# Kernel optimization log

Hardware: AMD Instinct MI355X
Metric: run time of the kernel (lower is better)

The kernel has to match this reference:

```python
import jax, jax.numpy as jnp
import numpy as np

N = 50000
E = 800000
NUM_GRAPHS = 128
X_IN, HID, EDGE_DIM = 64, 64, 16


def setup_inputs() -> dict:
    key = jax.random.key(0)
    ks = jax.random.split(key, 9)
    s = 0.05
    inp = {
        'x': jax.random.normal(ks[0], (N, X_IN), jnp.float32),
        'edge_index': jax.random.randint(ks[1], (2, E), 0, N, dtype=jnp.int32),
        'edge_attr': jax.random.normal(ks[2], (E, EDGE_DIM), jnp.float32),
        'batch': jnp.sort(jax.random.randint(ks[3], (N,), 0, NUM_GRAPHS, dtype=jnp.int32)),
        'w_fc1': jax.random.normal(ks[4], (EDGE_DIM, 1), jnp.float32) * s,
        'b_fc1': jnp.zeros((1,), jnp.float32),
    }
    dims = [(X_IN, HID), (HID, HID * 2), (HID * 2, HID)]
    for i, (din, dout) in enumerate(dims):
        k1, k2, k3 = jax.random.split(ks[5 + i], 3)
        inp[f'w1_{i}'] = jax.random.normal(k1, (din, dout), jnp.float32) * s
        inp[f'b1_{i}'] = jnp.zeros((dout,), jnp.float32)
        inp[f'w2_{i}'] = jax.random.normal(k2, (din, dout), jnp.float32) * s
        inp[f'w3_{i}'] = jax.random.normal(k3, (din, dout), jnp.float32) * s
        inp[f'b3_{i}'] = jnp.zeros((dout,), jnp.float32)
    return inp


def leconv(x, src, dst, ew, w1, b1, w2, w3, b3):
    # PyG LEConv: out_i = lin3(x_i) + sum_{j->i} e_ji * (lin1(x_j) - lin2(x_i))
    a = x @ w1 + b1          # lin1 (bias=True)   [N, out]
    b = x @ w2               # lin2 (bias=False)  [N, out]
    msg = ew[:, None] * (a[src] - b[dst])          # [E, out]
    agg = jax.ops.segment_sum(msg, dst, num_segments=N)
    return agg + x @ w3 + b3  # lin3 (bias=True)


def reference(x, edge_index, edge_attr, batch,
              w_fc1, b_fc1,
              w1_0, b1_0, w2_0, w3_0, b3_0,
              w1_1, b1_1, w2_1, w3_1, b3_1,
              w1_2, b1_2, w2_2, w3_2, b3_2):
    src, dst = edge_index[0], edge_index[1]
    ew = (edge_attr @ w_fc1 + b_fc1)[:, 0]         # fc1(edge_attr).squeeze(-1) -> [E]
    h = jax.nn.elu(leconv(x, src, dst, ew, w1_0, b1_0, w2_0, w3_0, b3_0))
    h = jax.nn.elu(leconv(h, src, dst, ew, w1_1, b1_1, w2_1, w3_1, b3_1))
    h = jax.nn.elu(leconv(h, src, dst, ew, w1_2, b1_2, w2_2, w3_2, b3_2))
    # global max pool over nodes of each graph -> [NUM_GRAPHS, HID]
    return jax.ops.segment_max(h, batch, num_segments=NUM_GRAPHS)
```

## Files before the change

### kernel.cpp

```cpp
#include <hip/hip_runtime.h>
#include <math.h>

#define N_NODES 50000
#define N_EDGES 800000
#define NUM_GRAPHS_ 128
#define SCAN_NB 98
#define NPASS 8
#define NODES_PER_PASS 6250
#define HCHUNKS 128
#define EDGES_PER_CHUNK 6250
#define HWORDS 12500
#define TS_BPH 196

typedef unsigned short u16;
typedef unsigned int u32;
typedef __attribute__((ext_vector_type(8))) short bf16x8;
typedef __attribute__((ext_vector_type(4))) float f32x4;

__device__ __forceinline__ float elu_f(float v) {
    return v > 0.f ? v : (__expf(v) - 1.f);
}
__device__ __forceinline__ u16 f2bf(float f) {
    u32 u = __float_as_uint(f);
    u += 0x7FFFu + ((u >> 16) & 1u);
    return (u16)(u >> 16);
}
__device__ __forceinline__ float bf2f(u16 h) {
    return __uint_as_float(((u32)h) << 16);
}
__device__ __forceinline__ void bfpair(u32 v, float& lo, float& hi) {
    lo = __uint_as_float(v << 16);
    hi = __uint_as_float(v & 0xFFFF0000u);
}
__device__ __forceinline__ u32 packbf(float lo, float hi) {
    return (u32)f2bf(lo) | ((u32)f2bf(hi) << 16);
}

__global__ void prep_kernel(const float* __restrict__ edge_attr,
                            const float* __restrict__ w_fc1,
                            const float* __restrict__ b_fc1,
                            const int* __restrict__ edge_index,
                            float* __restrict__ ew,
                            u16* __restrict__ dst16,
                            const float* __restrict__ x, u16* __restrict__ xb,
                            const float* __restrict__ w3_0, const float* __restrict__ w1_0, const float* __restrict__ w2_0,
                            const float* __restrict__ w3_1, const float* __restrict__ w1_1, const float* __restrict__ w2_1,
                            const float* __restrict__ w3_2, const float* __restrict__ w1_2, const float* __restrict__ w2_2,
                            u16* __restrict__ bp0, u16* __restrict__ bp1, u16* __restrict__ bp2) {
    const int b = blockIdx.x;
    if (b < 3125) {
        const int e = b * 256 + threadIdx.x;
        const float4* ea = (const float4*)(edge_attr + (size_t)e * 16);
        const float4* wf = (const float4*)w_fc1;
        float acc = b_fc1[0];
#pragma unroll
        for (int i = 0; i < 4; i++) {
            float4 a = ea[i], w = wf[i];
            acc += a.x * w.x + a.y * w.y + a.z * w.z + a.w * w.w;
        }
        ew[e] = acc;
        dst16[e] = (u16)edge_index[N_EDGES + e];
    } else if (b < 6250) {
        const int g = (b - 3125) * 256 + threadIdx.x;
        float4 v = ((const float4*)x)[g];
        uint2 o;
        o.x = packbf(v.x, v.y);
        o.y = packbf(v.z, v.w);
        ((uint2*)xb)[g] = o;
    } else {
        const int t = (b - 6250) * 256 + threadIdx.x;
        u16 buf[8];
        if (t < 4608) {
            int DOUT, lid;
            const float *w3, *w1, *w2;
            u16* bp;
            if (t < 1536) { DOUT = 64;  lid = t;        w3 = w3_0; w1 = w1_0; w2 = w2_0; bp = bp0; }
            else          { DOUT = 128; lid = t - 1536; w3 = w3_1; w1 = w1_1; w2 = w2_1; bp = bp1; }
            const int NT = DOUT / 16;
            const int lane = lid & 63;
            const int fragid = lid >> 6;
            const int chunk = fragid / NT;
            const int ntile = fragid % NT;
            const int n = ntile * 16 + (lane & 15);
            const int kbase = chunk * 32 + (lane >> 4) * 8;
#pragma unroll
            for (int j = 0; j < 8; j++) {
                int k = kbase + j;
                int region = k / 64;
                int kk = k - region * 64;
                float v = (region == 0) ? w3[kk * DOUT + n]
                        : (region == 1) ? w1[kk * DOUT + n]
                                        : -w2[kk * DOUT + n];
                buf[j] = f2bf(v);
            }
            *(bf16x8*)(bp + ((size_t)lid << 3)) = *(bf16x8*)buf;
        } else if (t < 7680) {
            const int lid = t - 4608;
            const int NT = 12;
            const int lane = lid & 63;
            const int fragid = lid >> 6;
            const int chunk = fragid / NT;
            const int ntile = fragid % NT;
            const int n = ntile * 16 + (lane & 15);
            const int kbase = chunk * 32 + (lane >> 4) * 8;
#pragma unroll
            for (int j = 0; j < 8; j++) {
                int k = kbase + j;
                float v = (n < 64)  ? w3_2[k * 64 + n]
                        : (n < 128) ? -w2_2[k * 64 + (n - 64)]
                                    : w1_2[k * 64 + (n - 128)];
                buf[j] = f2bf(v);
            }
            *(bf16x8*)(bp2 + ((size_t)lid << 3)) = *(bf16x8*)buf;
        }
    }
}

__global__ __launch_bounds__(256) void deg_hist_kernel(const u16* __restrict__ dst16,
                                                       u32* __restrict__ partial) {
    __shared__ u32 bins[HWORDS];
    const int c = blockIdx.x >> 1;
    const int p = blockIdx.x & 1;
    const int t = threadIdx.x;
    for (int i = t; i < HWORDS; i += 256) bins[i] = 0;
    __syncthreads();
    const int base = c * EDGES_PER_CHUNK;
    const int nlo = p * 25000;
    for (int i = t; i < EDGES_PER_CHUNK; i += 256) {
        const int b = (int)dst16[base + i] - nlo;
        if ((unsigned)b < 25000u)
            atomicAdd(&bins[b >> 1], 1u << ((b & 1) * 16));
    }
    __syncthreads();
    u32* outp = partial + (size_t)blockIdx.x * HWORDS;
    for (int i = t; i < HWORDS; i += 256) outp[i] = bins[i];
}

__global__ __launch_bounds__(256) void scan_chunks_kernel(const u32* __restrict__ partial,
                                                          u32* __restrict__ prefpack,
                                                          u32* __restrict__ degpack) {
    __shared__ u32 qsums[4][64];
    const int t = threadIdx.x;
    const int p = (blockIdx.x >= TS_BPH) ? 1 : 0;
    const int wh0 = (blockIdx.x - p * TS_BPH) << 6;
    const int wl = t & 63;
    const int cq = t >> 6;
    const int wh = wh0 + wl;
    const bool ok = wh < HWORDS;

    u32 vals[32];
#pragma unroll
    for (int i = 0; i < 32; i++) {
        const int c = cq * 32 + i;
        vals[i] = ok ? partial[(size_t)((c << 1) + p) * HWORDS + wh] : 0u;
    }
    u32 s = 0;
#pragma unroll
    for (int i = 0; i < 32; i++) s += vals[i];
    qsums[cq][wl] = s;
    __syncthreads();
    u32 run = 0;
#pragma unroll
    for (int j = 0; j < 4; j++)
        if (j < cq) run += qsums[j][wl];

    if (ok) {
        const int g = p * HWORDS + wh;
#pragma unroll
        for (int i = 0; i < 32; i++) {
            const int c = cq * 32 + i;
            prefpack[(size_t)c * 25000 + g] = run;
            run += vals[i];
        }
        if (cq == 3) degpack[g] = run;
    }
}

__global__ __launch_bounds__(256) void scan1_kernel(const u32* __restrict__ degpack,
                                                    int* __restrict__ rowptr,
                                                    int* __restrict__ blk_sums) {
    __shared__ int sh[256];
    const int t = threadIdx.x;
    const int base = blockIdx.x * 512;
    const int i0 = base + 2 * t, i1 = i0 + 1;
    int d0 = 0, d1 = 0;
    if (i0 < N_NODES) {
        u32 v = degpack[i0 >> 1];
        d0 = (int)(v & 0xFFFFu);
        d1 = (int)(v >> 16);
    }
    const int pair = d0 + d1;
    int v = pair;
    sh[t] = v;
    __syncthreads();
#pragma unroll
    for (int off = 1; off < 256; off <<= 1) {
        int add = (t >= off) ? sh[t - off] : 0;
        __syncthreads();
        v += add;
        sh[t] = v;
        __syncthreads();
    }
    const int excl = v - pair;
    if (i0 < N_NODES) rowptr[i0] = excl;
    if (i1 < N_NODES) rowptr[i1] = excl + d0;
    if (t == 255) blk_sums[blockIdx.x] = v;
}

__global__ __launch_bounds__(128) void scan2_kernel(const int* __restrict__ blk_sums,
                                                    int* __restrict__ blk_offs,
                                                    int* __restrict__ rowptr) {
    __shared__ int sh[128];
    const int t = threadIdx.x;
    const int orig = (t < SCAN_NB) ? blk_sums[t] : 0;
    int v = orig;
    sh[t] = v;
    __syncthreads();
#pragma unroll
    for (int off = 1; off < 128; off <<= 1) {
        int add = (t >= off) ? sh[t - off] : 0;
        __syncthreads();
        v += add;
        sh[t] = v;
        __syncthreads();
    }
    if (t < SCAN_NB) blk_offs[t] = v - orig;
    if (t == 127) rowptr[N_NODES] = v;
}

__global__ void scan3_kernel(int* __restrict__ rowptr,
                             const int* __restrict__ blk_offs) {
    int i = blockIdx.x * blockDim.x + threadIdx.x;
    if (i >= N_NODES) return;
    rowptr[i] += blk_offs[i >> 9];
}

__global__ __launch_bounds__(256) void place_kernel(const int* __restrict__ edge_index,
                                                    const float* __restrict__ ew,
                                                    const u16* __restrict__ dst16,
                                                    const int* __restrict__ rowptr,
                                                    const u32* __restrict__ prefpack,
                                                    int2* __restrict__ csr) {
    __shared__ int lcur[NODES_PER_PASS];
    const int pass = blockIdx.x & (NPASS - 1);
    const int c = blockIdx.x >> 3;
    const int lo = pass * NODES_PER_PASS;
    const int t = threadIdx.x;
    for (int i = t; i < NODES_PER_PASS; i += 256) lcur[i] = 0;
    __syncthreads();
    const int base = c * EDGES_PER_CHUNK;
    for (int i = t; i < EDGES_PER_CHUNK; i += 256) {
        const int e = base + i;
        const int d = (int)dst16[e];
        const int dl = d - lo;
        if ((unsigned)dl < (unsigned)NODES_PER_PASS) {
            u32 pw = prefpack[(size_t)c * 25000 + (d >> 1)];
            int pref = (int)((pw >> ((d & 1) * 16)) & 0xFFFFu);
            int lpos = atomicAdd(&lcur[dl], 1);
            int2 ent;
            ent.x = edge_index[e];
            ent.y = __float_as_int(ew[e]);
            csr[rowptr[d] + pref + lpos] = ent;
        }
    }
}

template <int DIN, bool WRITE_C>
__global__ __launch_bounds__(256) void gather_kernel(
    const u16* __restrict__ xb, const int* __restrict__ rowptr,
    const int2* __restrict__ csr, u16* __restrict__ sb,
    u16* __restrict__ chb, float* __restrict__ c) {
    constexpr int CG = DIN / 4;
    constexpr int EG = 64 / CG;
    const int gid = blockIdx.x * 256 + threadIdx.x;
    const int node = gid >> 6;
    if (node >= N_NODES) return;
    const int lane = threadIdx.x & 63;
    const int cg = lane & (CG - 1);
    const int eg = lane / CG;
    const int beg = rowptr[node];
    const int end = rowptr[node + 1];
    const uint2* x2 = (const uint2*)xb;

    float a0 = 0.f, a1 = 0.f, a2 = 0.f, a3 = 0.f;
    float b0 = 0.f, b1 = 0.f, b2 = 0.f, b3 = 0.f;
    float wsum = 0.f;

    int p = beg + eg;
    for (; p + EG < end; p += 2 * EG) {
        int2 e0 = csr[p];
        int2 e1 = csr[p + EG];
        float w0 = __int_as_float(e0.y);
        float w1 = __int_as_float(e1.y);
        uint2 v0 = x2[(size_t)e0.x * CG + cg];
        uint2 v1 = x2[(size_t)e1.x * CG + cg];
        float f0, f1, f2, f3, g0, g1, g2, g3;
        bfpair(v0.x, f0, f1); bfpair(v0.y, f2, f3);
        bfpair(v1.x, g0, g1); bfpair(v1.y, g2, g3);
        a0 += w0 * f0; a1 += w0 * f1; a2 += w0 * f2; a3 += w0 * f3;
        b0 += w1 * g0; b1 += w1 * g1; b2 += w1 * g2; b3 += w1 * g3;
        wsum += w0 + w1;
    }
    if (p < end) {
        int2 e0 = csr[p];
        float w0 = __int_as_float(e0.y);
        uint2 v0 = x2[(size_t)e0.x * CG + cg];
        float f0, f1, f2, f3;
        bfpair(v0.x, f0, f1); bfpair(v0.y, f2, f3);
        a0 += w0 * f0; a1 += w0 * f1; a2 += w0 * f2; a3 += w0 * f3;
        wsum += w0;
    }
    a0 += b0; a1 += b1; a2 += b2; a3 += b3;

#pragma unroll
    for (int off = 32; off >= CG; off >>= 1) {
        a0 += __shfl_xor(a0, off);
        a1 += __shfl_xor(a1, off);
        a2 += __shfl_xor(a2, off);
        a3 += __shfl_xor(a3, off);
        wsum += __shfl_xor(wsum, off);
    }

    if (lane < CG) {
        uint2 so;
        so.x = packbf(a0, a1);
        so.y = packbf(a2, a3);
        ((uint2*)sb)[(size_t)node * CG + cg] = so;
        const float cn = WRITE_C ? wsum : c[node];
        uint2 hv = x2[(size_t)node * CG + cg];
        float h0, h1, h2, h3;
        bfpair(hv.x, h0, h1); bfpair(hv.y, h2, h3);
        uint2 co;
        co.x = packbf(cn * h0, cn * h1);
        co.y = packbf(cn * h2, cn * h3);
        ((uint2*)chb)[(size_t)node * CG + cg] = co;
    }
    if (WRITE_C && lane == 0) c[node] = wsum;
}

template <int DIN, int DOUT>
__global__ __launch_bounds__(256) void gemm_mfma(
    const u16* __restrict__ hb, const u16* __restrict__ sb,
    const u16* __restrict__ chb, const u16* __restrict__ Bp,
    const float* __restrict__ cvec, const float* __restrict__ bias1,
    const float* __restrict__ bias3, u16* __restrict__ outp) {
    constexpr int CH = DIN / 32;
    constexpr int CHUNKS = 3 * CH;
    constexpr int NT = DOUT / 16;
    const int tid = threadIdx.x;
    const int wv = tid >> 6;
    const int lane = tid & 63;
    const int l15 = lane & 15;
    const int q = lane >> 4;
    const int mhalf = wv & 1;
    const int nhalf = wv >> 1;
    const int row_base = blockIdx.x * 64 + mhalf * 32;
    const int nt0 = blockIdx.y * 4 + nhalf * 2;

    const int r0 = min(row_base + l15, N_NODES - 1);
    const int r1 = min(row_base + 16 + l15, N_NODES - 1);
    const int qo = q * 8;

    f32x4 acc00 = {0.f, 0.f, 0.f, 0.f};
    f32x4 acc01 = {0.f, 0.f, 0.f, 0.f};
    f32x4 acc10 = {0.f, 0.f, 0.f, 0.f};
    f32x4 acc11 = {0.f, 0.f, 0.f, 0.f};

#pragma unroll
    for (int chunk = 0; chunk < CHUNKS; chunk++) {
        const int region = chunk / CH;
        const int koff = (chunk - region * CH) * 32 + qo;
        const u16* A = (region == 0) ? hb : (region == 1) ? sb : chb;
        bf16x8 a0 = *(const bf16x8*)(A + (size_t)r0 * DIN + koff);
        bf16x8 a1 = *(const bf16x8*)(A + (size_t)r1 * DIN + koff);
        const u16* bp = Bp + (((size_t)(chunk * NT + nt0) * 64 + lane) << 3);
        bf16x8 bf0 = *(const bf16x8*)bp;
        bf16x8 bf1 = *(const bf16x8*)(bp + 64 * 8);
        acc00 = __builtin_amdgcn_mfma_f32_16x16x32_bf16(a0, bf0, acc00, 0, 0, 0);
        acc01 = __builtin_amdgcn_mfma_f32_16x16x32_bf16(a0, bf1, acc01, 0, 0, 0);
        acc10 = __builtin_amdgcn_mfma_f32_16x16x32_bf16(a1, bf0, acc10, 0, 0, 0);
        acc11 = __builtin_amdgcn_mfma_f32_16x16x32_bf16(a1, bf1, acc11, 0, 0, 0);
    }

#pragma unroll
    for (int ni = 0; ni < 2; ni++) {
        const int col = (nt0 + ni) * 16 + l15;
        const float B3 = bias3[col];
        const float B1 = bias1[col];
        const f32x4 am0 = ni ? acc01 : acc00;
        const f32x4 am1 = ni ? acc11 : acc10;
#pragma unroll
        for (int mi = 0; mi < 2; mi++) {
            const f32x4 av = mi ? am1 : am0;
#pragma unroll
            for (int reg = 0; reg < 4; reg++) {
                const int row = row_base + mi * 16 + q * 4 + reg;
                if (row < N_NODES) {
                    const float cv = cvec[row];
                    const float val = av[reg] + B3 + cv * B1;
                    outp[(size_t)row * DOUT + col] = f2bf(elu_f(val));
                }
            }
        }
    }
}

__global__ __launch_bounds__(256) void gemm_l1_fused(
    const u16* __restrict__ hb, const u16* __restrict__ sb,
    const u16* __restrict__ chb, const u16* __restrict__ Bp1,
    const u16* __restrict__ Bp2, const float* __restrict__ cvec,
    const float* __restrict__ bias1, const float* __restrict__ bias3,
    u16* __restrict__ zuy) {
    __shared__ u16 ht[64][136];
    const int tid = threadIdx.x;
    const int wv = tid >> 6;
    const int lane = tid & 63;
    const int l15 = lane & 15;
    const int q = lane >> 4;
    const int mhalf = wv & 1;
    const int nhalf = wv >> 1;
    const int row_base = blockIdx.x * 64 + mhalf * 32;
    const int r0 = min(row_base + l15, N_NODES - 1);
    const int r1 = min(row_base + 16 + l15, N_NODES - 1);
    const int qo = q * 8;

    {
        const int nt0 = nhalf * 4;
        f32x4 acc[2][4] = {};
#pragma unroll
        for (int chunk = 0; chunk < 6; chunk++) {
            const int region = chunk / 2;
            const int koff = (chunk - region * 2) * 32 + qo;
            const u16* A = (region == 0) ? hb : (region == 1) ? sb : chb;
            bf16x8 a0 = *(const bf16x8*)(A + (size_t)r0 * 64 + koff);
            bf16x8 a1 = *(const bf16x8*)(A + (size_t)r1 * 64 + koff);
#pragma unroll
            for (int ni = 0; ni < 4; ni++) {
                bf16x8 bf = *(const bf16x8*)(Bp1 + (((size_t)(chunk * 8 + nt0 + ni) * 64 + lane) << 3));
                acc[0][ni] = __builtin_amdgcn_mfma_f32_16x16x32_bf16(a0, bf, acc[0][ni], 0, 0, 0);
                acc[1][ni] = __builtin_amdgcn_mfma_f32_16x16x32_bf16(a1, bf, acc[1][ni], 0, 0, 0);
            }
        }
#pragma unroll
        for (int ni = 0; ni < 4; ni++) {
            const int col = (nt0 + ni) * 16 + l15;
            const float B3 = bias3[col];
            const float B1 = bias1[col];
#pragma unroll
            for (int mi = 0; mi < 2; mi++) {
#pragma unroll
                for (int reg = 0; reg < 4; reg++) {
                    const int lrow = mhalf * 32 + mi * 16 + q * 4 + reg;
                    const int grow = blockIdx.x * 64 + lrow;
                    const float cv = cvec[min(grow, N_NODES - 1)];
                    ht[lrow][col] = f2bf(elu_f(acc[mi][ni][reg] + B3 + cv * B1));
                }
            }
        }
    }
    __syncthreads();

    {
        const int nt2 = nhalf * 6;
        f32x4 acc[2][6] = {};
#pragma unroll
        for (int chunk = 0; chunk < 4; chunk++) {
            const int koff = chunk * 32 + qo;
            bf16x8 a0 = *(const bf16x8*)(&ht[mhalf * 32 + l15][koff]);
            bf16x8 a1 = *(const bf16x8*)(&ht[mhalf * 32 + 16 + l15][koff]);
#pragma unroll
            for (int ni = 0; ni < 6; ni++) {
                bf16x8 bf = *(const bf16x8*)(Bp2 + (((size_t)(chunk * 12 + nt2 + ni) * 64 + lane) << 3));
                acc[0][ni] = __builtin_amdgcn_mfma_f32_16x16x32_bf16(a0, bf, acc[0][ni], 0, 0, 0);
                acc[1][ni] = __builtin_amdgcn_mfma_f32_16x16x32_bf16(a1, bf, acc[1][ni], 0, 0, 0);
            }
        }
#pragma unroll
        for (int ni = 0; ni < 6; ni++) {
            const int col = (nt2 + ni) * 16 + l15;
#pragma unroll
            for (int mi = 0; mi < 2; mi++) {
#pragma unroll
                for (int reg = 0; reg < 4; reg++) {
                    const int row = row_base + mi * 16 + q * 4 + reg;
                    if (row < N_NODES)
                        zuy[(size_t)row * 192 + col] = f2bf(acc[mi][ni][reg]);
                }
            }
        }
    }
}

__global__ __launch_bounds__(256) void gather2_kernel(
    const u16* __restrict__ zuy, const int* __restrict__ rowptr,
    const int2* __restrict__ csr, const float* __restrict__ c,
    const float* __restrict__ bias1, const float* __restrict__ bias3,
    u16* __restrict__ h3) {
    constexpr int CG = 16, EG = 4;
    const int gid = blockIdx.x * 256 + threadIdx.x;
    const int node = gid >> 6;
    if (node >= N_NODES) return;
    const int lane = threadIdx.x & 63;
    const int cg = lane & (CG - 1);
    const int eg = lane >> 4;
    const int beg = rowptr[node];
    const int end = rowptr[node + 1];

    float a0 = 0.f, a1 = 0.f, a2 = 0.f, a3 = 0.f;
    float b0 = 0.f, b1 = 0.f, b2 = 0.f, b3 = 0.f;

    int p = beg + eg;
    for (; p + EG < end; p += 2 * EG) {
        int2 e0 = csr[p];
        int2 e1 = csr[p + EG];
        float w0 = __int_as_float(e0.y);
        float w1 = __int_as_float(e1.y);
        uint2 v0 = ((const uint2*)(zuy + (size_t)e0.x * 192 + 128))[cg];
        uint2 v1 = ((const uint2*)(zuy + (size_t)e1.x * 192 + 128))[cg];
        float f0, f1, f2, f3, g0, g1, g2, g3;
        bfpair(v0.x, f0, f1); bfpair(v0.y, f2, f3);
        bfpair(v1.x, g0, g1); bfpair(v1.y, g2, g3);
        a0 += w0 * f0; a1 += w0 * f1; a2 += w0 * f2; a3 += w0 * f3;
        b0 += w1 * g0; b1 += w1 * g1; b2 += w1 * g2; b3 += w1 * g3;
    }
    if (p < end) {
        int2 e0 = csr[p];
        float w0 = __int_as_float(e0.y);
        uint2 v0 = ((const uint2*)(zuy + (size_t)e0.x * 192 + 128))[cg];
        float f0, f1, f2, f3;
        bfpair(v0.x, f0, f1); bfpair(v0.y, f2, f3);
        a0 += w0 * f0; a1 += w0 * f1; a2 += w0 * f2; a3 += w0 * f3;
    }
    a0 += b0; a1 += b1; a2 += b2; a3 += b3;

#pragma unroll
    for (int off = 32; off >= CG; off >>= 1) {
        a0 += __shfl_xor(a0, off);
        a1 += __shfl_xor(a1, off);
        a2 += __shfl_xor(a2, off);
        a3 += __shfl_xor(a3, off);
    }

    if (lane < CG) {
        const float cn = c[node];
        const u16* zr = zuy + (size_t)node * 192;
        uint2 zv = ((const uint2*)zr)[cg];
        uint2 uv = ((const uint2*)(zr + 64))[cg];
        float z0, z1, z2, z3, u0, u1, u2, u3;
        bfpair(zv.x, z0, z1); bfpair(zv.y, z2, z3);
        bfpair(uv.x, u0, u1); bfpair(uv.y, u2, u3);
        const float4 b3v = *(const float4*)(bias3 + cg * 4);
        const float4 b1v = *(const float4*)(bias1 + cg * 4);
        float o0 = elu_f(z0 + cn * u0 + a0 + b3v.x + cn * b1v.x);
        float o1 = elu_f(z1 + cn * u1 + a1 + b3v.y + cn * b1v.y);
        float o2 = elu_f(z2 + cn * u2 + a2 + b3v.z + cn * b1v.z);
        float o3 = elu_f(z3 + cn * u3 + a3 + b3v.w + cn * b1v.w);
        uint2 o;
        o.x = packbf(o0, o1);
        o.y = packbf(o2, o3);
        ((uint2*)h3)[(size_t)node * CG + cg] = o;
    }
}

__global__ void pool_kernel(const u16* __restrict__ h,
                            const int* __restrict__ batch,
                            float* __restrict__ out) {
    const int g = blockIdx.x;
    const int tid = threadIdx.x;
    int lo = 0, hi = N_NODES;
    while (lo < hi) { int mid = (lo + hi) >> 1; if (batch[mid] < g) lo = mid + 1; else hi = mid; }
    const int beg = lo;
    lo = beg; hi = N_NODES;
    while (lo < hi) { int mid = (lo + hi) >> 1; if (batch[mid] < g + 1) lo = mid + 1; else hi = mid; }
    const int end = lo;

    __shared__ float red[256];
    const int col = tid & 63;
    const int rg = tid >> 6;
    float m = -3.0e38f;
    for (int r = beg + rg; r < end; r += 4) m = fmaxf(m, bf2f(h[(size_t)r * 64 + col]));
    red[tid] = m;
    __syncthreads();
    if (tid < 64) {
        m = fmaxf(fmaxf(red[tid], red[tid + 64]), fmaxf(red[tid + 128], red[tid + 192]));
        out[g * 64 + tid] = m;
    }
}

extern "C" void kernel_launch(void* const* d_in, const int* in_sizes, int n_in,
                              void* d_out, int out_size, void* d_ws, size_t ws_size,
                              hipStream_t stream) {
    const float* x = (const float*)d_in[0];
    const int* ei = (const int*)d_in[1];
    const float* ea = (const float*)d_in[2];
    const int* batch = (const int*)d_in[3];
    const float* wfc = (const float*)d_in[4];
    const float* bfc = (const float*)d_in[5];
    const float* w1_0 = (const float*)d_in[6];
    const float* b1_0 = (const float*)d_in[7];
    const float* w2_0 = (const float*)d_in[8];
    const float* w3_0 = (const float*)d_in[9];
    const float* b3_0 = (const float*)d_in[10];
    const float* w1_1 = (const float*)d_in[11];
    const float* b1_1 = (const float*)d_in[12];
    const float* w2_1 = (const float*)d_in[13];
    const float* w3_1 = (const float*)d_in[14];
    const float* b3_1 = (const float*)d_in[15];
    const float* w1_2 = (const float*)d_in[16];
    const float* b1_2 = (const float*)d_in[17];
    const float* w2_2 = (const float*)d_in[18];
    const float* w3_2 = (const float*)d_in[19];
    const float* b3_2 = (const float*)d_in[20];
    float* out = (float*)d_out;

    char* ws = (char*)d_ws;
    float* ew      = (float*)(ws);
    float* c       = (float*)(ws + 3200000);
    int*   rowptr  = (int*)  (ws + 3800000);
    int2*  csr     = (int2*) (ws + 4000128);
    u16*   xb      = (u16*)  (ws + 10400128);
    u16*   sb      = (u16*)  (ws + 16800128);
    u16*   chb     = (u16*)  (ws + 29600128);
    u16*   h1      = (u16*)  (ws + 42400128);
    u16*   zuy     = (u16*)  (ws + 48800128);
    u16*   bp0     = (u16*)  (ws + 68000128);
    u16*   bp1     = (u16*)  (ws + 68024704);
    u16*   bp2     = (u16*)  (ws + 68073856);
    int* blk_sums  = (int*)  (ws + 68123008);
    int* blk_offs  = (int*)  (ws + 68123520);
    u16* dst16   = chb;
    u32* degpack = (u32*)(ws + 31600128);
    u32* partial = (u32*)sb;
    u32* prefpack = (u32*)zuy;
    u16* h3 = xb;

    prep_kernel<<<6280, 256, 0, stream>>>(ea, wfc, bfc, ei, ew, dst16, x, xb,
                                          w3_0, w1_0, w2_0, w3_1, w1_1, w2_1,
                                          w3_2, w1_2, w2_2, bp0, bp1, bp2);
    deg_hist_kernel<<<HCHUNKS * 2, 256, 0, stream>>>(dst16, partial);
    scan_chunks_kernel<<<TS_BPH * 2, 256, 0, stream>>>(partial, prefpack, degpack);
    scan1_kernel<<<SCAN_NB, 256, 0, stream>>>(degpack, rowptr, blk_sums);
    scan2_kernel<<<1, 128, 0, stream>>>(blk_sums, blk_offs, rowptr);
    scan3_kernel<<<(N_NODES + 255) / 256, 256, 0, stream>>>(rowptr, blk_offs);
    place_kernel<<<HCHUNKS * NPASS, 256, 0, stream>>>(ei, ew, dst16, rowptr, prefpack, csr);

    const int RB = (N_NODES + 63) / 64;
    const int GBLK = (N_NODES * 64 + 255) / 256;

    gather_kernel<64, true><<<GBLK, 256, 0, stream>>>(xb, rowptr, csr, sb, chb, c);
    gemm_mfma<64, 64><<<dim3(RB, 1), 256, 0, stream>>>(xb, sb, chb, bp0, c, b1_0, b3_0, h1);

    gather_kernel<64, false><<<GBLK, 256, 0, stream>>>(h1, rowptr, csr, sb, chb, c);
    gemm_l1_fused<<<RB, 256, 0, stream>>>(h1, sb, chb, bp1, bp2, c, b1_1, b3_1, zuy);

    gather2_kernel<<<GBLK, 256, 0, stream>>>(zuy, rowptr, csr, c, b1_2, b3_2, h3);

    pool_kernel<<<NUM_GRAPHS_, 256, 0, stream>>>(h3, batch, out);
}
```

Measured before the change: 329.2 us.

## Fuse neighbor gather with MFMA GEMM in shared memory for layers 0 and 1

Merges the per-layer gather kernels with their following MFMA GEMM kernels. Each 1024-thread block gathers 64 nodes into a shared-memory A tile (h, s, c*h), then runs the GEMM from LDS. This removes the global round trip of the sb/chb intermediates and two kernel launches. Workspace is remapped because those buffers are gone. It also halves the place kernel's pass count, so each block uses a larger shared cursor array. In exchange, 16 waves now share each block's gather, and the larger LDS footprint may lower occupancy.

```diff
diff --git a/kernel.cpp b/kernel.cpp
--- a/kernel.cpp
+++ b/kernel.cpp
@@ -5,8 +5,8 @@
 #define N_EDGES 800000
 #define NUM_GRAPHS_ 128
 #define SCAN_NB 98
-#define NPASS 8
-#define NODES_PER_PASS 6250
+#define NPASS 4
+#define NODES_PER_PASS 12500
 #define HCHUNKS 128
 #define EDGES_PER_CHUNK 6250
 #define HWORDS 12500
@@ -243,7 +243,7 @@
                                                     int2* __restrict__ csr) {
     __shared__ int lcur[NODES_PER_PASS];
     const int pass = blockIdx.x & (NPASS - 1);
-    const int c = blockIdx.x >> 3;
+    const int c = blockIdx.x >> 2;
     const int lo = pass * NODES_PER_PASS;
     const int t = threadIdx.x;
     for (int i = t; i < NODES_PER_PASS; i += 256) lcur[i] = 0;
@@ -265,227 +265,242 @@
     }
 }
 
-template <int DIN, bool WRITE_C>
-__global__ __launch_bounds__(256) void gather_kernel(
+__global__ __launch_bounds__(1024) void fused_l0(
     const u16* __restrict__ xb, const int* __restrict__ rowptr,
-    const int2* __restrict__ csr, u16* __restrict__ sb,
-    u16* __restrict__ chb, float* __restrict__ c) {
-    constexpr int CG = DIN / 4;
-    constexpr int EG = 64 / CG;
-    const int gid = blockIdx.x * 256 + threadIdx.x;
-    const int node = gid >> 6;
-    if (node >= N_NODES) return;
-    const int lane = threadIdx.x & 63;
-    const int cg = lane & (CG - 1);
-    const int eg = lane / CG;
-    const int beg = rowptr[node];
-    const int end = rowptr[node + 1];
-    const uint2* x2 = (const uint2*)xb;
-
-    float a0 = 0.f, a1 = 0.f, a2 = 0.f, a3 = 0.f;
-    float b0 = 0.f, b1 = 0.f, b2 = 0.f, b3 = 0.f;
-    float wsum = 0.f;
-
-    int p = beg + eg;
-    for (; p + EG < end; p += 2 * EG) {
-        int2 e0 = csr[p];
-        int2 e1 = csr[p + EG];
-        float w0 = __int_as_float(e0.y);
-        float w1 = __int_as_float(e1.y);
-        uint2 v0 = x2[(size_t)e0.x * CG + cg];
-        uint2 v1 = x2[(size_t)e1.x * CG + cg];
-        float f0, f1, f2, f3, g0, g1, g2, g3;
-        bfpair(v0.x, f0, f1); bfpair(v0.y, f2, f3);
-        bfpair(v1.x, g0, g1); bfpair(v1.y, g2, g3);
-        a0 += w0 * f0; a1 += w0 * f1; a2 += w0 * f2; a3 += w0 * f3;
-        b0 += w1 * g0; b1 += w1 * g1; b2 += w1 * g2; b3 += w1 * g3;
-        wsum += w0 + w1;
-    }
-    if (p < end) {
-        int2 e0 = csr[p];
-        float w0 = __int_as_float(e0.y);
-        uint2 v0 = x2[(size_t)e0.x * CG + cg];
-        float f0, f1, f2, f3;
-        bfpair(v0.x, f0, f1); bfpair(v0.y, f2, f3);
-        a0 += w0 * f0; a1 += w0 * f1; a2 += w0 * f2; a3 += w0 * f3;
-        wsum += w0;
-    }
-    a0 += b0; a1 += b1; a2 += b2; a3 += b3;
-
-#pragma unroll
-    for (int off = 32; off >= CG; off >>= 1) {
-        a0 += __shfl_xor(a0, off);
-        a1 += __shfl_xor(a1, off);
-        a2 += __shfl_xor(a2, off);
-        a3 += __shfl_xor(a3, off);
-        wsum += __shfl_xor(wsum, off);
-    }
-
-    if (lane < CG) {
-        uint2 so;
-        so.x = packbf(a0, a1);
-        so.y = packbf(a2, a3);
-        ((uint2*)sb)[(size_t)node * CG + cg] = so;
-        const float cn = WRITE_C ? wsum : c[node];
-        uint2 hv = x2[(size_t)node * CG + cg];
-        float h0, h1, h2, h3;
-        bfpair(hv.x, h0, h1); bfpair(hv.y, h2, h3);
-        uint2 co;
-        co.x = packbf(cn * h0, cn * h1);
-        co.y = packbf(cn * h2, cn * h3);
-        ((uint2*)chb)[(size_t)node * CG + cg] = co;
-    }
-    if (WRITE_C && lane == 0) c[node] = wsum;
-}
-
-template <int DIN, int DOUT>
-__global__ __launch_bounds__(256) void gemm_mfma(
-    const u16* __restrict__ hb, const u16* __restrict__ sb,
-    const u16* __restrict__ chb, const u16* __restrict__ Bp,
-    const float* __restrict__ cvec, const float* __restrict__ bias1,
-    const float* __restrict__ bias3, u16* __restrict__ outp) {
-    constexpr int CH = DIN / 32;
-    constexpr int CHUNKS = 3 * CH;
-    constexpr int NT = DOUT / 16;
+    const int2* __restrict__ csr, const u16* __restrict__ Bp0,
+    const float* __restrict__ bias1, const float* __restrict__ bias3,
+    float* __restrict__ cvec, u16* __restrict__ h1out) {
+    __shared__ u16 A[64][200];
+    __shared__ float csh[64];
     const int tid = threadIdx.x;
     const int wv = tid >> 6;
     const int lane = tid & 63;
+    const int node_base = blockIdx.x * 64;
+    const uint2* x2 = (const uint2*)xb;
+    const int cg = lane & 15;
+    const int eg = lane >> 4;
+
+    for (int k = 0; k < 4; k++) {
+        const int row = wv * 4 + k;
+        const int node = node_base + row;
+        float a0 = 0.f, a1 = 0.f, a2 = 0.f, a3 = 0.f;
+        float b0 = 0.f, b1 = 0.f, b2 = 0.f, b3 = 0.f;
+        float wsum = 0.f;
+        if (node < N_NODES) {
+            const int beg = rowptr[node];
+            const int end = rowptr[node + 1];
+            int p = beg + eg;
+            for (; p + 4 < end; p += 8) {
+                int2 e0 = csr[p];
+                int2 e1 = csr[p + 4];
+                float w0 = __int_as_float(e0.y);
+                float w1 = __int_as_float(e1.y);
+                uint2 v0 = x2[(size_t)e0.x * 16 + cg];
+                uint2 v1 = x2[(size_t)e1.x * 16 + cg];
+                float f0, f1, f2, f3, g0, g1, g2, g3;
+                bfpair(v0.x, f0, f1); bfpair(v0.y, f2, f3);
+                bfpair(v1.x, g0, g1); bfpair(v1.y, g2, g3);
+                a0 += w0 * f0; a1 += w0 * f1; a2 += w0 * f2; a3 += w0 * f3;
+                b0 += w1 * g0; b1 += w1 * g1; b2 += w1 * g2; b3 += w1 * g3;
+                wsum += w0 + w1;
+            }
+            if (p < end) {
+                int2 e0 = csr[p];
+                float w0 = __int_as_float(e0.y);
+                uint2 v0 = x2[(size_t)e0.x * 16 + cg];
+                float f0, f1, f2, f3;
+                bfpair(v0.x, f0, f1); bfpair(v0.y, f2, f3);
+                a0 += w0 * f0; a1 += w0 * f1; a2 += w0 * f2; a3 += w0 * f3;
+                wsum += w0;
+            }
+        }
+        a0 += b0; a1 += b1; a2 += b2; a3 += b3;
+#pragma unroll
+        for (int off = 32; off >= 16; off >>= 1) {
+            a0 += __shfl_xor(a0, off);
+            a1 += __shfl_xor(a1, off);
+            a2 += __shfl_xor(a2, off);
+            a3 += __shfl_xor(a3, off);
+            wsum += __shfl_xor(wsum, off);
+        }
+        if (lane < 16) {
+            const float cn = wsum;
+            uint2 hv = (node < N_NODES) ? x2[(size_t)node * 16 + cg] : (uint2){0u, 0u};
+            uint2 so;
+            so.x = packbf(a0, a1);
+            so.y = packbf(a2, a3);
+            *(uint2*)&A[row][cg * 4] = hv;
+            *(uint2*)&A[row][64 + cg * 4] = so;
+            float h0, h1f, h2f, h3f;
+            bfpair(hv.x, h0, h1f); bfpair(hv.y, h2f, h3f);
+            uint2 co;
+            co.x = packbf(cn * h0, cn * h1f);
+            co.y = packbf(cn * h2f, cn * h3f);
+            *(uint2*)&A[row][128 + cg * 4] = co;
+            if (cg == 0) {
+                csh[row] = cn;
+                if (node < N_NODES) cvec[node] = cn;
+            }
+        }
+    }
+    __syncthreads();
+
     const int l15 = lane & 15;
     const int q = lane >> 4;
-    const int mhalf = wv & 1;
-    const int nhalf = wv >> 1;
-    const int row_base = blockIdx.x * 64 + mhalf * 32;
-    const int nt0 = blockIdx.y * 4 + nhalf * 2;
-
-    const int r0 = min(row_base + l15, N_NODES - 1);
-    const int r1 = min(row_base + 16 + l15, N_NODES - 1);
     const int qo = q * 8;
-
-    f32x4 acc00 = {0.f, 0.f, 0.f, 0.f};
-    f32x4 acc01 = {0.f, 0.f, 0.f, 0.f};
-    f32x4 acc10 = {0.f, 0.f, 0.f, 0.f};
-    f32x4 acc11 = {0.f, 0.f, 0.f, 0.f};
-
-#pragma unroll
-    for (int chunk = 0; chunk < CHUNKS; chunk++) {
-        const int region = chunk / CH;
-        const int koff = (chunk - region * CH) * 32 + qo;
-        const u16* A = (region == 0) ? hb : (region == 1) ? sb : chb;
-        bf16x8 a0 = *(const bf16x8*)(A + (size_t)r0 * DIN + koff);
-        bf16x8 a1 = *(const bf16x8*)(A + (size_t)r1 * DIN + koff);
-        const u16* bp = Bp + (((size_t)(chunk * NT + nt0) * 64 + lane) << 3);
-        bf16x8 bf0 = *(const bf16x8*)bp;
-        bf16x8 bf1 = *(const bf16x8*)(bp + 64 * 8);
-        acc00 = __builtin_amdgcn_mfma_f32_16x16x32_bf16(a0, bf0, acc00, 0, 0, 0);
-        acc01 = __builtin_amdgcn_mfma_f32_16x16x32_bf16(a0, bf1, acc01, 0, 0, 0);
-        acc10 = __builtin_amdgcn_mfma_f32_16x16x32_bf16(a1, bf0, acc10, 0, 0, 0);
-        acc11 = __builtin_amdgcn_mfma_f32_16x16x32_bf16(a1, bf1, acc11, 0, 0, 0);
-    }
-
-#pragma unroll
-    for (int ni = 0; ni < 2; ni++) {
-        const int col = (nt0 + ni) * 16 + l15;
-        const float B3 = bias3[col];
-        const float B1 = bias1[col];
-        const f32x4 am0 = ni ? acc01 : acc00;
-        const f32x4 am1 = ni ? acc11 : acc10;
-#pragma unroll
-        for (int mi = 0; mi < 2; mi++) {
-            const f32x4 av = mi ? am1 : am0;
-#pragma unroll
-            for (int reg = 0; reg < 4; reg++) {
-                const int row = row_base + mi * 16 + q * 4 + reg;
-                if (row < N_NODES) {
-                    const float cv = cvec[row];
-                    const float val = av[reg] + B3 + cv * B1;
-                    outp[(size_t)row * DOUT + col] = f2bf(elu_f(val));
-                }
-            }
-        }
-    }
-}
-
-__global__ __launch_bounds__(256) void gemm_l1_fused(
-    const u16* __restrict__ hb, const u16* __restrict__ sb,
-    const u16* __restrict__ chb, const u16* __restrict__ Bp1,
-    const u16* __restrict__ Bp2, const float* __restrict__ cvec,
-    const float* __restrict__ bias1, const float* __restrict__ bias3,
-    u16* __restrict__ zuy) {
+    const int mt = wv >> 2, nt = wv & 3;
+    f32x4 acc = {0.f, 0.f, 0.f, 0.f};
+#pragma unroll
+    for (int chunk = 0; chunk < 6; chunk++) {
+        bf16x8 a = *(const bf16x8*)&A[mt * 16 + l15][chunk * 32 + qo];
+        bf16x8 b = *(const bf16x8*)(Bp0 + (((size_t)(chunk * 4 + nt) * 64 + lane) << 3));
+        acc = __builtin_amdgcn_mfma_f32_16x16x32_bf16(a, b, acc, 0, 0, 0);
+    }
+    const int col = nt * 16 + l15;
+    const float B3 = bias3[col];
+    const float B1 = bias1[col];
+#pragma unroll
+    for (int reg = 0; reg < 4; reg++) {
+        const int lrow = mt * 16 + q * 4 + reg;
+        const int row = node_base + lrow;
+        if (row < N_NODES) {
+            const float val = acc[reg] + B3 + csh[lrow] * B1;
+            h1out[(size_t)row * 64 + col] = f2bf(elu_f(val));
+        }
+    }
+}
+
+__global__ __launch_bounds__(1024) void fused_l1(
+    const u16* __restrict__ h1in, const int* __restrict__ rowptr,
+    const int2* __restrict__ csr, const u16* __restrict__ Bp1,
+    const u16* __restrict__ Bp2, const float* __restrict__ bias1,
+    const float* __restrict__ bias3, u16* __restrict__ zuy) {
+    __shared__ u16 A[64][200];
     __shared__ u16 ht[64][136];
+    __shared__ float csh[64];
     const int tid = threadIdx.x;
     const int wv = tid >> 6;
     const int lane = tid & 63;
+    const int node_base = blockIdx.x * 64;
+    const uint2* x2 = (const uint2*)h1in;
+    const int cg = lane & 15;
+    const int eg = lane >> 4;
+
+    for (int k = 0; k < 4; k++) {
+        const int row = wv * 4 + k;
+        const int node = node_base + row;
+        float a0 = 0.f, a1 = 0.f, a2 = 0.f, a3 = 0.f;
+        float b0 = 0.f, b1 = 0.f, b2 = 0.f, b3 = 0.f;
+        float wsum = 0.f;
+        if (node < N_NODES) {
+            const int beg = rowptr[node];
+            const int end = rowptr[node + 1];
+            int p = beg + eg;
+            for (; p + 4 < end; p += 8) {
+                int2 e0 = csr[p];
+                int2 e1 = csr[p + 4];
+                float w0 = __int_as_float(e0.y);
+                float w1 = __int_as_float(e1.y);
+                uint2 v0 = x2[(size_t)e0.x * 16 + cg];
+                uint2 v1 = x2[(size_t)e1.x * 16 + cg];
+                float f0, f1, f2, f3, g0, g1, g2, g3;
+                bfpair(v0.x, f0, f1); bfpair(v0.y, f2, f3);
+                bfpair(v1.x, g0, g1); bfpair(v1.y, g2, g3);
+                a0 += w0 * f0; a1 += w0 * f1; a2 += w0 * f2; a3 += w0 * f3;
+                b0 += w1 * g0; b1 += w1 * g1; b2 += w1 * g2; b3 += w1 * g3;
+                wsum += w0 + w1;
+            }
+            if (p < end) {
+                int2 e0 = csr[p];
+                float w0 = __int_as_float(e0.y);
+                uint2 v0 = x2[(size_t)e0.x * 16 + cg];
+                float f0, f1, f2, f3;
+                bfpair(v0.x, f0, f1); bfpair(v0.y, f2, f3);
+                a0 += w0 * f0; a1 += w0 * f1; a2 += w0 * f2; a3 += w0 * f3;
+                wsum += w0;
+            }
+        }
+        a0 += b0; a1 += b1; a2 += b2; a3 += b3;
+#pragma unroll
+        for (int off = 32; off >= 16; off >>= 1) {
+            a0 += __shfl_xor(a0, off);
+            a1 += __shfl_xor(a1, off);
+            a2 += __shfl_xor(a2, off);
+            a3 += __shfl_xor(a3, off);
+            wsum += __shfl_xor(wsum, off);
+        }
+        if (lane < 16) {
+            const float cn = wsum;
+            uint2 hv = (node < N_NODES) ? x2[(size_t)node * 16 + cg] : (uint2){0u, 0u};
+            uint2 so;
+            so.x = packbf(a0, a1);
+            so.y = packbf(a2, a3);
+            *(uint2*)&A[row][cg * 4] = hv;
+            *(uint2*)&A[row][64 + cg * 4] = so;
+            float h0, h1f, h2f, h3f;
+            bfpair(hv.x, h0, h1f); bfpair(hv.y, h2f, h3f);
+            uint2 co;
+            co.x = packbf(cn * h0, cn * h1f);
+            co.y = packbf(cn * h2f, cn * h3f);
+            *(uint2*)&A[row][128 + cg * 4] = co;
+            if (cg == 0) csh[row] = cn;
+        }
+    }
+    __syncthreads();
+
     const int l15 = lane & 15;
     const int q = lane >> 4;
-    const int mhalf = wv & 1;
-    const int nhalf = wv >> 1;
-    const int row_base = blockIdx.x * 64 + mhalf * 32;
-    const int r0 = min(row_base + l15, N_NODES - 1);
-    const int r1 = min(row_base + 16 + l15, N_NODES - 1);
     const int qo = q * 8;
 
     {
-        const int nt0 = nhalf * 4;
-        f32x4 acc[2][4] = {};
+        const int mt = wv >> 2;
+        const int nt0 = (wv & 3) * 2;
+        f32x4 acc0 = {0.f, 0.f, 0.f, 0.f};
+        f32x4 acc1 = {0.f, 0.f, 0.f, 0.f};
 #pragma unroll
         for (int chunk = 0; chunk < 6; chunk++) {
-            const int region = chunk / 2;
-            const int koff = (chunk - region * 2) * 32 + qo;
-            const u16* A = (region == 0) ? hb : (region == 1) ? sb : chb;
-            bf16x8 a0 = *(const bf16x8*)(A + (size_t)r0 * 64 + koff);
-            bf16x8 a1 = *(const bf16x8*)(A + (size_t)r1 * 64 + koff);
-#pragma unroll
-            for (int ni = 0; ni < 4; ni++) {
-                bf16x8 bf = *(const bf16x8*)(Bp1 + (((size_t)(chunk * 8 + nt0 + ni) * 64 + lane) << 3));
-                acc[0][ni] = __builtin_amdgcn_mfma_f32_16x16x32_bf16(a0, bf, acc[0][ni], 0, 0, 0);
-                acc[1][ni] = __builtin_amdgcn_mfma_f32_16x16x32_bf16(a1, bf, acc[1][ni], 0, 0, 0);
-            }
-        }
-#pragma unroll
-        for (int ni = 0; ni < 4; ni++) {
+            bf16x8 a = *(const bf16x8*)&A[mt * 16 + l15][chunk * 32 + qo];
+            bf16x8 bf0 = *(const bf16x8*)(Bp1 + (((size_t)(chunk * 8 + nt0) * 64 + lane) << 3));
+            bf16x8 bf1 = *(const bf16x8*)(Bp1 + (((size_t)(chunk * 8 + nt0 + 1) * 64 + lane) << 3));
+            acc0 = __builtin_amdgcn_mfma_f32_16x16x32_bf16(a, bf0, acc0, 0, 0, 0);
+            acc1 = __builtin_amdgcn_mfma_f32_16x16x32_bf16(a, bf1, acc1, 0, 0, 0);
+        }
+#pragma unroll
+        for (int ni = 0; ni < 2; ni++) {
             const int col = (nt0 + ni) * 16 + l15;
             const float B3 = bias3[col];
             const float B1 = bias1[col];
-#pragma unroll
-            for (int mi = 0; mi < 2; mi++) {
-#pragma unroll
-                for (int reg = 0; reg < 4; reg++) {
-                    const int lrow = mhalf * 32 + mi * 16 + q * 4 + reg;
-                    const int grow = blockIdx.x * 64 + lrow;
-                    const float cv = cvec[min(grow, N_NODES - 1)];
-                    ht[lrow][col] = f2bf(elu_f(acc[mi][ni][reg] + B3 + cv * B1));
-                }
+            const f32x4 av = ni ? acc1 : acc0;
+#pragma unroll
+            for (int reg = 0; reg < 4; reg++) {
+                const int lrow = mt * 16 + q * 4 + reg;
+                ht[lrow][col] = f2bf(elu_f(av[reg] + B3 + csh[lrow] * B1));
             }
         }
     }
     __syncthreads();
 
     {
-        const int nt2 = nhalf * 6;
-        f32x4 acc[2][6] = {};
+        const int mt = wv >> 2;
+        const int ntb = (wv & 3) * 3;
+        f32x4 acc[3] = {};
 #pragma unroll
         for (int chunk = 0; chunk < 4; chunk++) {
-            const int koff = chunk * 32 + qo;
-            bf16x8 a0 = *(const bf16x8*)(&ht[mhalf * 32 + l15][koff]);
-            bf16x8 a1 = *(const bf16x8*)(&ht[mhalf * 32 + 16 + l15][koff]);
-#pragma unroll
-            for (int ni = 0; ni < 6; ni++) {
-                bf16x8 bf = *(const bf16x8*)(Bp2 + (((size_t)(chunk * 12 + nt2 + ni) * 64 + lane) << 3));
-                acc[0][ni] = __builtin_amdgcn_mfma_f32_16x16x32_bf16(a0, bf, acc[0][ni], 0, 0, 0);
-                acc[1][ni] = __builtin_amdgcn_mfma_f32_16x16x32_bf16(a1, bf, acc[1][ni], 0, 0, 0);
-            }
-        }
-#pragma unroll
-        for (int ni = 0; ni < 6; ni++) {
-            const int col = (nt2 + ni) * 16 + l15;
-#pragma unroll
-            for (int mi = 0; mi < 2; mi++) {
-#pragma unroll
-                for (int reg = 0; reg < 4; reg++) {
-                    const int row = row_base + mi * 16 + q * 4 + reg;
-                    if (row < N_NODES)
-                        zuy[(size_t)row * 192 + col] = f2bf(acc[mi][ni][reg]);
-                }
+            bf16x8 a = *(const bf16x8*)&ht[mt * 16 + l15][chunk * 32 + qo];
+#pragma unroll
+            for (int j = 0; j < 3; j++) {
+                bf16x8 b = *(const bf16x8*)(Bp2 + (((size_t)(chunk * 12 + ntb + j) * 64 + lane) << 3));
+                acc[j] = __builtin_amdgcn_mfma_f32_16x16x32_bf16(a, b, acc[j], 0, 0, 0);
+            }
+        }
+#pragma unroll
+        for (int j = 0; j < 3; j++) {
+            const int col = (ntb + j) * 16 + l15;
+#pragma unroll
+            for (int reg = 0; reg < 4; reg++) {
+                const int row = node_base + mt * 16 + q * 4 + reg;
+                if (row < N_NODES)
+                    zuy[(size_t)row * 192 + col] = f2bf(acc[j][reg]);
             }
         }
     }
@@ -619,8 +634,9 @@
     int*   rowptr  = (int*)  (ws + 3800000);
     int2*  csr     = (int2*) (ws + 4000128);
     u16*   xb      = (u16*)  (ws + 10400128);
-    u16*   sb      = (u16*)  (ws + 16800128);
-    u16*   chb     = (u16*)  (ws + 29600128);
+    u32*   partial = (u32*)  (ws + 16800128);
+    u16*   dst16   = (u16*)  (ws + 29600128);
+    u32*   degpack = (u32*)  (ws + 31600128);
     u16*   h1      = (u16*)  (ws + 42400128);
     u16*   zuy     = (u16*)  (ws + 48800128);
     u16*   bp0     = (u16*)  (ws + 68000128);
@@ -628,9 +644,6 @@
     u16*   bp2     = (u16*)  (ws + 68073856);
     int* blk_sums  = (int*)  (ws + 68123008);
     int* blk_offs  = (int*)  (ws + 68123520);
-    u16* dst16   = chb;
-    u32* degpack = (u32*)(ws + 31600128);
-    u32* partial = (u32*)sb;
     u32* prefpack = (u32*)zuy;
     u16* h3 = xb;
 
@@ -647,11 +660,9 @@
     const int RB = (N_NODES + 63) / 64;
     const int GBLK = (N_NODES * 64 + 255) / 256;
 
-    gather_kernel<64, true><<<GBLK, 256, 0, stream>>>(xb, rowptr, csr, sb, chb, c);
-    gemm_mfma<64, 64><<<dim3(RB, 1), 256, 0, stream>>>(xb, sb, chb, bp0, c, b1_0, b3_0, h1);
-
-    gather_kernel<64, false><<<GBLK, 256, 0, stream>>>(h1, rowptr, csr, sb, chb, c);
-    gemm_l1_fused<<<RB, 256, 0, stream>>>(h1, sb, chb, bp1, bp2, c, b1_1, b3_1, zuy);
+    fused_l0<<<RB, 1024, 0, stream>>>(xb, rowptr, csr, bp0, b1_0, b3_0, c, h1);
+
+    fused_l1<<<RB, 1024, 0, stream>>>(h1, rowptr, csr, bp1, bp2, b1_1, b3_1, zuy);
 
     gather2_kernel<<<GBLK, 256, 0, stream>>>(zuy, rowptr, csr, c, b1_2, b3_2, h3);
 
```

Result: faster. 318.5 us (-3.3%).
